# Optimization experiments

Measured on AMD Instinct MI355X. Metric: run time of the kernel, lower is better.

The kernel has to match this reference:

```python
import jax, jax.numpy as jnp
import numpy as np

D_QK = 32  # out_channels // 8


def conv1x1(x, w, b):
    # x: [B,C,H,W], w: [O,C], b: [O] -> [B,O,H,W]
    return jnp.einsum('bchw,oc->bohw', x, w) + b[None, :, None, None]


def setup_inputs() -> dict:
    key = jax.random.key(0)
    ks = jax.random.split(key, 10)
    B, C, H, W = 4, 256, 64, 64
    in_ch, out_ch, attn_ch = 512, 256, 256
    s_in = 1.0 / np.sqrt(in_ch)
    s_at = 1.0 / np.sqrt(attn_ch)
    return {
        'ef': jax.random.normal(ks[0], (B, C, H, W), jnp.float32),
        'sf': jax.random.normal(ks[1], (B, C, H, W), jnp.float32),
        'Attn': jax.random.normal(ks[2], (B, attn_ch, H, W), jnp.float32),
        'Qw': jax.random.uniform(ks[3], (D_QK, in_ch), jnp.float32, -s_in, s_in),
        'Qb': jax.random.uniform(ks[4], (D_QK,), jnp.float32, -s_in, s_in),
        'Kw': jax.random.uniform(ks[5], (D_QK, attn_ch), jnp.float32, -s_at, s_at),
        'Kb': jax.random.uniform(ks[6], (D_QK,), jnp.float32, -s_at, s_at),
        'Vw': jax.random.uniform(ks[7], (out_ch, in_ch), jnp.float32, -s_in, s_in),
        'Vb': jax.random.uniform(ks[8], (out_ch,), jnp.float32, -s_in, s_in),
        'gamma': jnp.ones((1,), jnp.float32) * 0.25,
    }


def reference(ef, sf, Attn, Qw, Qb, Kw, Kb, Vw, Vb, gamma):
    B, C, H, W = ef.shape
    N = H * W
    x = jnp.concatenate((ef, sf), axis=1)  # [B, 2C, H, W]
    q = conv1x1(x, Qw, Qb).reshape(B, D_QK, N)         # [B, d, N]
    k = conv1x1(Attn, Kw, Kb).reshape(B, D_QK, N)      # [B, d, N]
    # scores[b, m, n] = sum_d q[b, d, m] * k[b, d, n]  (no 1/sqrt(d) scale)
    scores = jnp.einsum('bdm,bdn->bmn', q, k)
    attn = jax.nn.softmax(scores, axis=-1)             # [B, N, N]
    v = conv1x1(x, Vw, Vb).reshape(B, C, N)            # [B, C, N]
    # out[b, c, m] = sum_n v[b, c, n] * attn[b, m, n]
    out = jnp.einsum('bcn,bmn->bcm', v, attn).reshape(B, C, H, W)
    return gamma[0] * out + ef
```

## Files before the change

### kernel.cpp

```cpp
#include <hip/hip_runtime.h>
#include <hip/hip_bf16.h>

typedef short bf16x8 __attribute__((ext_vector_type(8)));
typedef float f32x4 __attribute__((ext_vector_type(4)));

#define MFMA16(a, b, c) __builtin_amdgcn_mfma_f32_16x16x32_bf16(a, b, c, 0, 0, 0)

#define NB 4
#define NC 256
#define NSP 4096
#define LOG2E 1.4426950408889634f

__device__ __forceinline__ unsigned short f2bf(float f) {
    return (unsigned short)((__float_as_uint(f) + 0x8000u) >> 16);
}
__device__ __forceinline__ unsigned pk2bf(float hi, float lo) {
    return __builtin_amdgcn_perm(__float_as_uint(hi) + 0x8000u,
                                 __float_as_uint(lo) + 0x8000u, 0x07060302u);
}

__global__ __launch_bounds__(256) void prep_w(
    const float* __restrict__ Qw, const float* __restrict__ Kw,
    const float* __restrict__ Vw,
    unsigned short* __restrict__ Qwbf, unsigned short* __restrict__ Kwbf,
    unsigned short* __restrict__ Vwbf)
{
    int i = blockIdx.x * 256 + threadIdx.x;
    {
        const float4* vs = (const float4*)(Vw + (size_t)i * 8);
        float4 a = vs[0], c = vs[1];
        int4 st;
        st.x = (int)pk2bf(a.y, a.x); st.y = (int)pk2bf(a.w, a.z);
        st.z = (int)pk2bf(c.y, c.x); st.w = (int)pk2bf(c.w, c.z);
        *(int4*)(Vwbf + (size_t)i * 8) = st;
    }
    if (i < 2048) {
        const float4* qs = (const float4*)(Qw + (size_t)i * 8);
        float4 a = qs[0], c = qs[1];
        int4 st;
        st.x = (int)pk2bf(a.y, a.x); st.y = (int)pk2bf(a.w, a.z);
        st.z = (int)pk2bf(c.y, c.x); st.w = (int)pk2bf(c.w, c.z);
        *(int4*)(Qwbf + (size_t)i * 8) = st;
    }
    if (i < 1024) {
        const float4* ks = (const float4*)(Kw + (size_t)i * 8);
        float4 a = ks[0], c = ks[1];
        int4 st;
        st.x = (int)pk2bf(a.y, a.x); st.y = (int)pk2bf(a.w, a.z);
        st.z = (int)pk2bf(c.y, c.x); st.w = (int)pk2bf(c.w, c.z);
        *(int4*)(Kwbf + (size_t)i * 8) = st;
    }
}

__global__ __launch_bounds__(256) void proj_q(
    const float* __restrict__ ef, const float* __restrict__ sf,
    const unsigned short* __restrict__ Qwbf, const float* __restrict__ Qb,
    unsigned short* __restrict__ qws)
{
    __shared__ __align__(16) unsigned short xt[32][72];

    int t = threadIdx.x;
    int w = t >> 6, lane = t & 63, quad = lane >> 4, l15 = lane & 15;
    int mt = blockIdx.x, b = blockIdx.y, m0 = mt * 32;
    int ci = t & 63, sm = t >> 6;
    int mi = w >> 1, oh = w & 1;

    f32x4 acc = {0.f, 0.f, 0.f, 0.f};

    for (int c = 0; c < 8; ++c) {
        const float* src = (c < 4 ? ef : sf) +
                           ((size_t)(b * NC) + (c & 3) * 64 + ci) * NSP + m0 + sm * 8;
        float4 x0 = *(const float4*)src;
        float4 x1 = *(const float4*)(src + 4);
        __syncthreads();
        unsigned short* xd = &xt[sm * 8][ci];
        xd[0]   = f2bf(x0.x); xd[72]  = f2bf(x0.y);
        xd[144] = f2bf(x0.z); xd[216] = f2bf(x0.w);
        xd[288] = f2bf(x1.x); xd[360] = f2bf(x1.y);
        xd[432] = f2bf(x1.z); xd[504] = f2bf(x1.w);
        __syncthreads();
        int ci0 = c * 64;
#pragma unroll
        for (int ks = 0; ks < 2; ++ks) {
            bf16x8 a  = *(const bf16x8*)&xt[mi * 16 + l15][ks * 32 + quad * 8];
            bf16x8 bq = *(const bf16x8*)(Qwbf + (size_t)(oh * 16 + l15) * 512 + ci0 + ks * 32 + quad * 8);
            acc = MFMA16(a, bq, acc);
        }
    }

    int o = oh * 16 + l15;
    float bb = Qb[o];
#pragma unroll
    for (int r = 0; r < 4; ++r) {
        int m = m0 + mi * 16 + quad * 4 + r;
        qws[((size_t)(b * NSP) + m) * 32 + o] = f2bf((acc[r] + bb) * LOG2E);
    }
}

__global__ __launch_bounds__(256) void proj_k(
    const float* __restrict__ attn,
    const unsigned short* __restrict__ Kwbf, const float* __restrict__ Kb,
    unsigned short* __restrict__ kws)
{
    __shared__ __align__(16) unsigned short xt[32][72];

    int t = threadIdx.x;
    int w = t >> 6, lane = t & 63, quad = lane >> 4, l15 = lane & 15;
    int mt = blockIdx.x, b = blockIdx.y, m0 = mt * 32;
    int ci = t & 63, sm = t >> 6;
    int mi = w >> 1, oh = w & 1;

    f32x4 acc = {0.f, 0.f, 0.f, 0.f};

    for (int c = 0; c < 4; ++c) {
        const float* src = attn + ((size_t)(b * NC) + c * 64 + ci) * NSP + m0 + sm * 8;
        float4 x0 = *(const float4*)src;
        float4 x1 = *(const float4*)(src + 4);
        __syncthreads();
        unsigned short* xd = &xt[sm * 8][ci];
        xd[0]   = f2bf(x0.x); xd[72]  = f2bf(x0.y);
        xd[144] = f2bf(x0.z); xd[216] = f2bf(x0.w);
        xd[288] = f2bf(x1.x); xd[360] = f2bf(x1.y);
        xd[432] = f2bf(x1.z); xd[504] = f2bf(x1.w);
        __syncthreads();
        int ci0 = c * 64;
#pragma unroll
        for (int ks = 0; ks < 2; ++ks) {
            bf16x8 a  = *(const bf16x8*)&xt[mi * 16 + l15][ks * 32 + quad * 8];
            bf16x8 bk = *(const bf16x8*)(Kwbf + (size_t)(oh * 16 + l15) * 256 + ci0 + ks * 32 + quad * 8);
            acc = MFMA16(a, bk, acc);
        }
    }

    int o = oh * 16 + l15;
    float bb = Kb[o];
#pragma unroll
    for (int r = 0; r < 4; ++r) {
        int m = m0 + mi * 16 + quad * 4 + r;
        kws[((size_t)(b * NSP) + m) * 32 + o] = f2bf(acc[r] + bb);
    }
}

__global__ __launch_bounds__(256) void proj_v(
    const float* __restrict__ ef, const float* __restrict__ sf,
    const unsigned short* __restrict__ Vwbf, const float* __restrict__ Vb,
    unsigned short* __restrict__ vws)
{
    __shared__ __align__(16) unsigned short xt[32][72];

    int t = threadIdx.x;
    int w = t >> 6, lane = t & 63, quad = lane >> 4, l15 = lane & 15;
    int mt = blockIdx.x, b = blockIdx.y, m0 = mt * 32;
    int ci = t & 63, sm = t >> 6;

    f32x4 zero = {0.f, 0.f, 0.f, 0.f};
    f32x4 acc[2][4];
#pragma unroll
    for (int mi = 0; mi < 2; ++mi)
#pragma unroll
        for (int ot = 0; ot < 4; ++ot) acc[mi][ot] = zero;

    for (int c = 0; c < 8; ++c) {
        const float* src = (c < 4 ? ef : sf) +
                           ((size_t)(b * NC) + (c & 3) * 64 + ci) * NSP + m0 + sm * 8;
        float4 x0 = *(const float4*)src;
        float4 x1 = *(const float4*)(src + 4);
        __syncthreads();
        unsigned short* xd = &xt[sm * 8][ci];
        xd[0]   = f2bf(x0.x); xd[72]  = f2bf(x0.y);
        xd[144] = f2bf(x0.z); xd[216] = f2bf(x0.w);
        xd[288] = f2bf(x1.x); xd[360] = f2bf(x1.y);
        xd[432] = f2bf(x1.z); xd[504] = f2bf(x1.w);
        __syncthreads();
        int ci0 = c * 64;
#pragma unroll
        for (int ks = 0; ks < 2; ++ks) {
            bf16x8 a0 = *(const bf16x8*)&xt[l15][ks * 32 + quad * 8];
            bf16x8 a1 = *(const bf16x8*)&xt[16 + l15][ks * 32 + quad * 8];
#pragma unroll
            for (int ot = 0; ot < 4; ++ot) {
                bf16x8 bv = *(const bf16x8*)(Vwbf + (size_t)(w * 64 + ot * 16 + l15) * 512 + ci0 + ks * 32 + quad * 8);
                acc[0][ot] = MFMA16(a0, bv, acc[0][ot]);
                acc[1][ot] = MFMA16(a1, bv, acc[1][ot]);
            }
        }
    }

#pragma unroll
    for (int ot = 0; ot < 4; ++ot) {
        int ch = w * 64 + ot * 16 + l15;
        float bias = Vb[ch];
        unsigned* vp = (unsigned*)(vws + ((size_t)((b * 128 + mt) * 256 + ch)) * 32);
#pragma unroll
        for (int r = 0; r < 4; ++r)
            vp[quad * 4 + r] = pk2bf(acc[1][ot][r] + bias, acc[0][ot][r] + bias);
    }
}

__global__ __launch_bounds__(512, 2) void attention(
    const unsigned short* __restrict__ qws, const unsigned short* __restrict__ kws,
    const unsigned short* __restrict__ vws, const float* __restrict__ ef,
    const float* __restrict__ gamma, float* __restrict__ out)
{
    __shared__ unsigned short Plds[2][2][64 * 72];
    __shared__ float mrg[256][68];
    __shared__ float denl[2][64];

    int t = threadIdx.x;
    int g = t >> 8, tl = t & 255;
    int w = tl >> 6, lane = tl & 63, quad = lane >> 4, l15 = lane & 15;
    int b = blockIdx.x >> 6, m0 = (blockIdx.x & 63) << 6;

    const unsigned short* kbase = kws + (size_t)(b * NSP) * 32;
    const unsigned short* vbase = vws + (size_t)(b * 128) * 8192;

    bf16x8 qf = *(const bf16x8*)(qws + ((size_t)(b * NSP) + m0 + w * 16 + l15) * 32 + quad * 8);

    f32x4 zero = {0.f, 0.f, 0.f, 0.f};
    f32x4 acc[4][4];
#pragma unroll
    for (int i = 0; i < 4; ++i)
#pragma unroll
        for (int j = 0; j < 4; ++j) acc[i][j] = zero;
    float lp0 = 0.f, lp1 = 0.f, lp2 = 0.f, lp3 = 0.f;

    int tt0 = g * 64;
    bf16x8 kf[4];
#pragma unroll
    for (int j = 0; j < 4; ++j)
        kf[j] = *(const bf16x8*)(kbase + (size_t)((tt0 + (j >> 1)) * 32 + (j & 1) * 16 + l15) * 32 + quad * 8);
    bf16x8 vf[2][4];
#pragma unroll
    for (int h = 0; h < 2; ++h)
#pragma unroll
        for (int cc = 0; cc < 4; ++cc)
            vf[h][cc] = *(const bf16x8*)(vbase + (size_t)(tt0 + h) * 8192 + (w * 64 + cc * 16 + l15) * 32 + quad * 8);

    for (int it = 0; it < 32; ++it) {
        int buf = it & 1;
        f32x4 s0 = MFMA16(qf, kf[0], zero);
        f32x4 s1 = MFMA16(qf, kf[1], zero);
        f32x4 s2 = MFMA16(qf, kf[2], zero);
        f32x4 s3 = MFMA16(qf, kf[3], zero);

        float e0[4], e1[4], e2[4], e3[4];
#pragma unroll
        for (int r = 0; r < 4; ++r) {
            e0[r] = __builtin_amdgcn_exp2f(s0[r]);
            e1[r] = __builtin_amdgcn_exp2f(s1[r]);
            e2[r] = __builtin_amdgcn_exp2f(s2[r]);
            e3[r] = __builtin_amdgcn_exp2f(s3[r]);
        }
        lp0 += (e0[0] + e1[0]) + (e2[0] + e3[0]);
        lp1 += (e0[1] + e1[1]) + (e2[1] + e3[1]);
        lp2 += (e0[2] + e1[2]) + (e2[2] + e3[2]);
        lp3 += (e0[3] + e1[3]) + (e2[3] + e3[3]);

        unsigned short* pd = &Plds[g][buf][(w * 16 + quad * 4) * 72 + 2 * l15];
#pragma unroll
        for (int r = 0; r < 4; ++r) {
            *(unsigned*)(pd + r * 72)      = pk2bf(e1[r], e0[r]);
            *(unsigned*)(pd + r * 72 + 32) = pk2bf(e3[r], e2[r]);
        }

        int itn = it + 1 < 32 ? it + 1 : 31;
        int ttn = tt0 + 2 * itn;
#pragma unroll
        for (int j = 0; j < 4; ++j)
            kf[j] = *(const bf16x8*)(kbase + (size_t)((ttn + (j >> 1)) * 32 + (j & 1) * 16 + l15) * 32 + quad * 8);
        bf16x8 vfn[2][4];
#pragma unroll
        for (int h = 0; h < 2; ++h)
#pragma unroll
            for (int cc = 0; cc < 4; ++cc)
                vfn[h][cc] = *(const bf16x8*)(vbase + (size_t)(ttn + h) * 8192 + (w * 64 + cc * 16 + l15) * 32 + quad * 8);

        __syncthreads();

#pragma unroll
        for (int h = 0; h < 2; ++h) {
            bf16x8 pa0 = *(const bf16x8*)&Plds[g][buf][(0  + l15) * 72 + h * 32 + quad * 8];
            bf16x8 pa1 = *(const bf16x8*)&Plds[g][buf][(16 + l15) * 72 + h * 32 + quad * 8];
            bf16x8 pa2 = *(const bf16x8*)&Plds[g][buf][(32 + l15) * 72 + h * 32 + quad * 8];
            bf16x8 pa3 = *(const bf16x8*)&Plds[g][buf][(48 + l15) * 72 + h * 32 + quad * 8];
#pragma unroll
            for (int cc = 0; cc < 4; ++cc) {
                acc[0][cc] = MFMA16(pa0, vf[h][cc], acc[0][cc]);
                acc[1][cc] = MFMA16(pa1, vf[h][cc], acc[1][cc]);
                acc[2][cc] = MFMA16(pa2, vf[h][cc], acc[2][cc]);
                acc[3][cc] = MFMA16(pa3, vf[h][cc], acc[3][cc]);
            }
        }
#pragma unroll
        for (int h = 0; h < 2; ++h)
#pragma unroll
            for (int cc = 0; cc < 4; ++cc) vf[h][cc] = vfn[h][cc];
    }

    lp0 += __shfl_xor(lp0, 1); lp0 += __shfl_xor(lp0, 2); lp0 += __shfl_xor(lp0, 4); lp0 += __shfl_xor(lp0, 8);
    lp1 += __shfl_xor(lp1, 1); lp1 += __shfl_xor(lp1, 2); lp1 += __shfl_xor(lp1, 4); lp1 += __shfl_xor(lp1, 8);
    lp2 += __shfl_xor(lp2, 1); lp2 += __shfl_xor(lp2, 2); lp2 += __shfl_xor(lp2, 4); lp2 += __shfl_xor(lp2, 8);
    lp3 += __shfl_xor(lp3, 1); lp3 += __shfl_xor(lp3, 2); lp3 += __shfl_xor(lp3, 4); lp3 += __shfl_xor(lp3, 8);
    if (l15 == 0) {
        int base = w * 16 + quad * 4;
        denl[g][base + 0] = lp0; denl[g][base + 1] = lp1;
        denl[g][base + 2] = lp2; denl[g][base + 3] = lp3;
    }
    if (g == 1) {
#pragma unroll
        for (int qc = 0; qc < 4; ++qc)
#pragma unroll
            for (int cc = 0; cc < 4; ++cc)
                *(f32x4*)&mrg[w * 64 + cc * 16 + l15][qc * 16 + quad * 4] = acc[qc][cc];
    }
    __syncthreads();

    if (g == 0) {
        float gam = gamma[0];
#pragma unroll
        for (int qc = 0; qc < 4; ++qc) {
            int qb = qc * 16 + quad * 4;
            float4 d0 = *(const float4*)&denl[0][qb];
            float4 d1 = *(const float4*)&denl[1][qb];
            float r0 = gam / (d0.x + d1.x), r1 = gam / (d0.y + d1.y);
            float r2 = gam / (d0.z + d1.z), r3 = gam / (d0.w + d1.w);
#pragma unroll
            for (int cc = 0; cc < 4; ++cc) {
                int ch = w * 64 + cc * 16 + l15;
                f32x4 part = *(const f32x4*)&mrg[ch][qb];
                size_t off = ((size_t)(b * NC + ch)) * NSP + m0 + qb;
                float4 e = *(const float4*)(ef + off);
                float4 o;
                o.x = (acc[qc][cc][0] + part[0]) * r0 + e.x;
                o.y = (acc[qc][cc][1] + part[1]) * r1 + e.y;
                o.z = (acc[qc][cc][2] + part[2]) * r2 + e.z;
                o.w = (acc[qc][cc][3] + part[3]) * r3 + e.w;
                *(float4*)(out + off) = o;
            }
        }
    }
}

extern "C" void kernel_launch(void* const* d_in, const int* in_sizes, int n_in,
                              void* d_out, int out_size, void* d_ws, size_t ws_size,
                              hipStream_t stream) {
    const float* ef    = (const float*)d_in[0];
    const float* sf    = (const float*)d_in[1];
    const float* attn  = (const float*)d_in[2];
    const float* Qw    = (const float*)d_in[3];
    const float* Qb    = (const float*)d_in[4];
    const float* Kw    = (const float*)d_in[5];
    const float* Kb    = (const float*)d_in[6];
    const float* Vw    = (const float*)d_in[7];
    const float* Vb    = (const float*)d_in[8];
    const float* gamma = (const float*)d_in[9];
    float* out = (float*)d_out;

    unsigned short* qws  = (unsigned short*)d_ws;
    unsigned short* kws  = qws + (size_t)4 * 4096 * 32;
    unsigned short* vws  = kws + (size_t)4 * 4096 * 32;
    unsigned short* Qwbf = vws + (size_t)4 * 128 * 256 * 32;
    unsigned short* Kwbf = Qwbf + 32 * 512;
    unsigned short* Vwbf = Kwbf + 32 * 256;

    hipLaunchKernelGGL(prep_w, dim3(64), dim3(256), 0, stream,
                       Qw, Kw, Vw, Qwbf, Kwbf, Vwbf);
    hipLaunchKernelGGL(proj_q, dim3(128, 4), dim3(256), 0, stream,
                       ef, sf, Qwbf, Qb, qws);
    hipLaunchKernelGGL(proj_k, dim3(128, 4), dim3(256), 0, stream,
                       attn, Kwbf, Kb, kws);
    hipLaunchKernelGGL(proj_v, dim3(128, 4), dim3(256), 0, stream,
                       ef, sf, Vwbf, Vb, vws);
    hipLaunchKernelGGL(attention, dim3(256), dim3(512), 0, stream,
                       qws, kws, vws, ef, gamma, out);
}
```

Measured before the change: 192.0 us.

## Fuse Q/V projections, prefetch inputs, split attention keys across four groups

Merges the Q and V projection kernels so ef/sf are read and converted to bf16 once, and adds register prefetch of the next channel chunk in the projection loops. The attention kernel grows to 1024 threads, with four warp groups each covering a quarter of the key range, and combines their partial sums through a two-stage LDS reduction that reuses the P buffer. It also raises wave priority around the PV MFMA block. The gain is more parallelism per block and less redundant input traffic, at the cost of higher register and LDS pressure and extra reduction syncs.

```diff
diff --git a/kernel.cpp b/kernel.cpp
--- a/kernel.cpp
+++ b/kernel.cpp
@@ -52,10 +52,11 @@
     }
 }
 
-__global__ __launch_bounds__(256) void proj_q(
+__global__ __launch_bounds__(256) void proj_qv(
     const float* __restrict__ ef, const float* __restrict__ sf,
     const unsigned short* __restrict__ Qwbf, const float* __restrict__ Qb,
-    unsigned short* __restrict__ qws)
+    const unsigned short* __restrict__ Vwbf, const float* __restrict__ Vb,
+    unsigned short* __restrict__ qws, unsigned short* __restrict__ vws)
 {
     __shared__ __align__(16) unsigned short xt[32][72];
 
@@ -65,13 +66,27 @@
     int ci = t & 63, sm = t >> 6;
     int mi = w >> 1, oh = w & 1;
 
-    f32x4 acc = {0.f, 0.f, 0.f, 0.f};
+    f32x4 zero = {0.f, 0.f, 0.f, 0.f};
+    f32x4 acc[2][4];
+#pragma unroll
+    for (int m = 0; m < 2; ++m)
+#pragma unroll
+        for (int ot = 0; ot < 4; ++ot) acc[m][ot] = zero;
+    f32x4 qacc = zero;
+
+    const float* s0p = ef + ((size_t)(b * NC) + ci) * NSP + m0 + sm * 8;
+    float4 x0 = *(const float4*)s0p;
+    float4 x1 = *(const float4*)(s0p + 4);
 
     for (int c = 0; c < 8; ++c) {
-        const float* src = (c < 4 ? ef : sf) +
-                           ((size_t)(b * NC) + (c & 3) * 64 + ci) * NSP + m0 + sm * 8;
-        float4 x0 = *(const float4*)src;
-        float4 x1 = *(const float4*)(src + 4);
+        float4 n0 = x0, n1 = x1;
+        if (c < 7) {
+            int cn = c + 1;
+            const float* sn = (cn < 4 ? ef : sf) +
+                              ((size_t)(b * NC) + (cn & 3) * 64 + ci) * NSP + m0 + sm * 8;
+            n0 = *(const float4*)sn;
+            n1 = *(const float4*)(sn + 4);
+        }
         __syncthreads();
         unsigned short* xd = &xt[sm * 8][ci];
         xd[0]   = f2bf(x0.x); xd[72]  = f2bf(x0.y);
@@ -82,18 +97,38 @@
         int ci0 = c * 64;
 #pragma unroll
         for (int ks = 0; ks < 2; ++ks) {
-            bf16x8 a  = *(const bf16x8*)&xt[mi * 16 + l15][ks * 32 + quad * 8];
+            bf16x8 a0 = *(const bf16x8*)&xt[l15][ks * 32 + quad * 8];
+            bf16x8 a1 = *(const bf16x8*)&xt[16 + l15][ks * 32 + quad * 8];
             bf16x8 bq = *(const bf16x8*)(Qwbf + (size_t)(oh * 16 + l15) * 512 + ci0 + ks * 32 + quad * 8);
-            acc = MFMA16(a, bq, acc);
-        }
-    }
-
-    int o = oh * 16 + l15;
-    float bb = Qb[o];
-#pragma unroll
-    for (int r = 0; r < 4; ++r) {
-        int m = m0 + mi * 16 + quad * 4 + r;
-        qws[((size_t)(b * NSP) + m) * 32 + o] = f2bf((acc[r] + bb) * LOG2E);
+            qacc = MFMA16(mi ? a1 : a0, bq, qacc);
+#pragma unroll
+            for (int ot = 0; ot < 4; ++ot) {
+                bf16x8 bv = *(const bf16x8*)(Vwbf + (size_t)(w * 64 + ot * 16 + l15) * 512 + ci0 + ks * 32 + quad * 8);
+                acc[0][ot] = MFMA16(a0, bv, acc[0][ot]);
+                acc[1][ot] = MFMA16(a1, bv, acc[1][ot]);
+            }
+        }
+        x0 = n0; x1 = n1;
+    }
+
+#pragma unroll
+    for (int ot = 0; ot < 4; ++ot) {
+        int ch = w * 64 + ot * 16 + l15;
+        float bias = Vb[ch];
+        unsigned* vp = (unsigned*)(vws + ((size_t)((b * 128 + mt) * 256 + ch)) * 32);
+#pragma unroll
+        for (int r = 0; r < 4; ++r)
+            vp[quad * 4 + r] = pk2bf(acc[1][ot][r] + bias, acc[0][ot][r] + bias);
+    }
+
+    {
+        int o = oh * 16 + l15;
+        float bb = Qb[o];
+#pragma unroll
+        for (int r = 0; r < 4; ++r) {
+            int m = m0 + mi * 16 + quad * 4 + r;
+            qws[((size_t)(b * NSP) + m) * 32 + o] = f2bf((qacc[r] + bb) * LOG2E);
+        }
     }
 }
 
@@ -112,10 +147,17 @@
 
     f32x4 acc = {0.f, 0.f, 0.f, 0.f};
 
+    const float* s0p = attn + ((size_t)(b * NC) + ci) * NSP + m0 + sm * 8;
+    float4 x0 = *(const float4*)s0p;
+    float4 x1 = *(const float4*)(s0p + 4);
+
     for (int c = 0; c < 4; ++c) {
-        const float* src = attn + ((size_t)(b * NC) + c * 64 + ci) * NSP + m0 + sm * 8;
-        float4 x0 = *(const float4*)src;
-        float4 x1 = *(const float4*)(src + 4);
+        float4 n0 = x0, n1 = x1;
+        if (c < 3) {
+            const float* sn = attn + ((size_t)(b * NC) + (c + 1) * 64 + ci) * NSP + m0 + sm * 8;
+            n0 = *(const float4*)sn;
+            n1 = *(const float4*)(sn + 4);
+        }
         __syncthreads();
         unsigned short* xd = &xt[sm * 8][ci];
         xd[0]   = f2bf(x0.x); xd[72]  = f2bf(x0.y);
@@ -130,6 +172,7 @@
             bf16x8 bk = *(const bf16x8*)(Kwbf + (size_t)(oh * 16 + l15) * 256 + ci0 + ks * 32 + quad * 8);
             acc = MFMA16(a, bk, acc);
         }
+        x0 = n0; x1 = n1;
     }
 
     int o = oh * 16 + l15;
@@ -141,70 +184,14 @@
     }
 }
 
-__global__ __launch_bounds__(256) void proj_v(
-    const float* __restrict__ ef, const float* __restrict__ sf,
-    const unsigned short* __restrict__ Vwbf, const float* __restrict__ Vb,
-    unsigned short* __restrict__ vws)
-{
-    __shared__ __align__(16) unsigned short xt[32][72];
-
-    int t = threadIdx.x;
-    int w = t >> 6, lane = t & 63, quad = lane >> 4, l15 = lane & 15;
-    int mt = blockIdx.x, b = blockIdx.y, m0 = mt * 32;
-    int ci = t & 63, sm = t >> 6;
-
-    f32x4 zero = {0.f, 0.f, 0.f, 0.f};
-    f32x4 acc[2][4];
-#pragma unroll
-    for (int mi = 0; mi < 2; ++mi)
-#pragma unroll
-        for (int ot = 0; ot < 4; ++ot) acc[mi][ot] = zero;
-
-    for (int c = 0; c < 8; ++c) {
-        const float* src = (c < 4 ? ef : sf) +
-                           ((size_t)(b * NC) + (c & 3) * 64 + ci) * NSP + m0 + sm * 8;
-        float4 x0 = *(const float4*)src;
-        float4 x1 = *(const float4*)(src + 4);
-        __syncthreads();
-        unsigned short* xd = &xt[sm * 8][ci];
-        xd[0]   = f2bf(x0.x); xd[72]  = f2bf(x0.y);
-        xd[144] = f2bf(x0.z); xd[216] = f2bf(x0.w);
-        xd[288] = f2bf(x1.x); xd[360] = f2bf(x1.y);
-        xd[432] = f2bf(x1.z); xd[504] = f2bf(x1.w);
-        __syncthreads();
-        int ci0 = c * 64;
-#pragma unroll
-        for (int ks = 0; ks < 2; ++ks) {
-            bf16x8 a0 = *(const bf16x8*)&xt[l15][ks * 32 + quad * 8];
-            bf16x8 a1 = *(const bf16x8*)&xt[16 + l15][ks * 32 + quad * 8];
-#pragma unroll
-            for (int ot = 0; ot < 4; ++ot) {
-                bf16x8 bv = *(const bf16x8*)(Vwbf + (size_t)(w * 64 + ot * 16 + l15) * 512 + ci0 + ks * 32 + quad * 8);
-                acc[0][ot] = MFMA16(a0, bv, acc[0][ot]);
-                acc[1][ot] = MFMA16(a1, bv, acc[1][ot]);
-            }
-        }
-    }
-
-#pragma unroll
-    for (int ot = 0; ot < 4; ++ot) {
-        int ch = w * 64 + ot * 16 + l15;
-        float bias = Vb[ch];
-        unsigned* vp = (unsigned*)(vws + ((size_t)((b * 128 + mt) * 256 + ch)) * 32);
-#pragma unroll
-        for (int r = 0; r < 4; ++r)
-            vp[quad * 4 + r] = pk2bf(acc[1][ot][r] + bias, acc[0][ot][r] + bias);
-    }
-}
-
-__global__ __launch_bounds__(512, 2) void attention(
+__global__ __launch_bounds__(1024, 4) void attention(
     const unsigned short* __restrict__ qws, const unsigned short* __restrict__ kws,
     const unsigned short* __restrict__ vws, const float* __restrict__ ef,
     const float* __restrict__ gamma, float* __restrict__ out)
 {
-    __shared__ unsigned short Plds[2][2][64 * 72];
-    __shared__ float mrg[256][68];
-    __shared__ float denl[2][64];
+    __shared__ __align__(16) unsigned short PldsRaw[4][2][64 * 72];
+    __shared__ __align__(16) float mrgA[256][68];
+    __shared__ float denl[4][64];
 
     int t = threadIdx.x;
     int g = t >> 8, tl = t & 255;
@@ -224,7 +211,7 @@
         for (int j = 0; j < 4; ++j) acc[i][j] = zero;
     float lp0 = 0.f, lp1 = 0.f, lp2 = 0.f, lp3 = 0.f;
 
-    int tt0 = g * 64;
+    int tt0 = g * 32;
     bf16x8 kf[4];
 #pragma unroll
     for (int j = 0; j < 4; ++j)
@@ -236,7 +223,7 @@
         for (int cc = 0; cc < 4; ++cc)
             vf[h][cc] = *(const bf16x8*)(vbase + (size_t)(tt0 + h) * 8192 + (w * 64 + cc * 16 + l15) * 32 + quad * 8);
 
-    for (int it = 0; it < 32; ++it) {
+    for (int it = 0; it < 16; ++it) {
         int buf = it & 1;
         f32x4 s0 = MFMA16(qf, kf[0], zero);
         f32x4 s1 = MFMA16(qf, kf[1], zero);
@@ -256,14 +243,14 @@
         lp2 += (e0[2] + e1[2]) + (e2[2] + e3[2]);
         lp3 += (e0[3] + e1[3]) + (e2[3] + e3[3]);
 
-        unsigned short* pd = &Plds[g][buf][(w * 16 + quad * 4) * 72 + 2 * l15];
+        unsigned short* pd = &PldsRaw[g][buf][(w * 16 + quad * 4) * 72 + 2 * l15];
 #pragma unroll
         for (int r = 0; r < 4; ++r) {
             *(unsigned*)(pd + r * 72)      = pk2bf(e1[r], e0[r]);
             *(unsigned*)(pd + r * 72 + 32) = pk2bf(e3[r], e2[r]);
         }
 
-        int itn = it + 1 < 32 ? it + 1 : 31;
+        int itn = it + 1 < 16 ? it + 1 : 15;
         int ttn = tt0 + 2 * itn;
 #pragma unroll
         for (int j = 0; j < 4; ++j)
@@ -277,12 +264,13 @@
 
         __syncthreads();
 
+        __builtin_amdgcn_s_setprio(1);
 #pragma unroll
         for (int h = 0; h < 2; ++h) {
-            bf16x8 pa0 = *(const bf16x8*)&Plds[g][buf][(0  + l15) * 72 + h * 32 + quad * 8];
-            bf16x8 pa1 = *(const bf16x8*)&Plds[g][buf][(16 + l15) * 72 + h * 32 + quad * 8];
-            bf16x8 pa2 = *(const bf16x8*)&Plds[g][buf][(32 + l15) * 72 + h * 32 + quad * 8];
-            bf16x8 pa3 = *(const bf16x8*)&Plds[g][buf][(48 + l15) * 72 + h * 32 + quad * 8];
+            bf16x8 pa0 = *(const bf16x8*)&PldsRaw[g][buf][(0  + l15) * 72 + h * 32 + quad * 8];
+            bf16x8 pa1 = *(const bf16x8*)&PldsRaw[g][buf][(16 + l15) * 72 + h * 32 + quad * 8];
+            bf16x8 pa2 = *(const bf16x8*)&PldsRaw[g][buf][(32 + l15) * 72 + h * 32 + quad * 8];
+            bf16x8 pa3 = *(const bf16x8*)&PldsRaw[g][buf][(48 + l15) * 72 + h * 32 + quad * 8];
 #pragma unroll
             for (int cc = 0; cc < 4; ++cc) {
                 acc[0][cc] = MFMA16(pa0, vf[h][cc], acc[0][cc]);
@@ -291,6 +279,7 @@
                 acc[3][cc] = MFMA16(pa3, vf[h][cc], acc[3][cc]);
             }
         }
+        __builtin_amdgcn_s_setprio(0);
 #pragma unroll
         for (int h = 0; h < 2; ++h)
 #pragma unroll
@@ -306,12 +295,43 @@
         denl[g][base + 0] = lp0; denl[g][base + 1] = lp1;
         denl[g][base + 2] = lp2; denl[g][base + 3] = lp3;
     }
+    __syncthreads();
+
+    float (*mrgB)[68] = (float (*)[68])&PldsRaw[0][0][0];
+
     if (g == 1) {
 #pragma unroll
         for (int qc = 0; qc < 4; ++qc)
 #pragma unroll
             for (int cc = 0; cc < 4; ++cc)
-                *(f32x4*)&mrg[w * 64 + cc * 16 + l15][qc * 16 + quad * 4] = acc[qc][cc];
+                *(f32x4*)&mrgA[w * 64 + cc * 16 + l15][qc * 16 + quad * 4] = acc[qc][cc];
+    }
+    if (g == 3) {
+#pragma unroll
+        for (int qc = 0; qc < 4; ++qc)
+#pragma unroll
+            for (int cc = 0; cc < 4; ++cc)
+                *(f32x4*)&mrgB[w * 64 + cc * 16 + l15][qc * 16 + quad * 4] = acc[qc][cc];
+    }
+    __syncthreads();
+
+    if (g == 0) {
+#pragma unroll
+        for (int qc = 0; qc < 4; ++qc)
+#pragma unroll
+            for (int cc = 0; cc < 4; ++cc)
+                acc[qc][cc] += *(const f32x4*)&mrgA[w * 64 + cc * 16 + l15][qc * 16 + quad * 4];
+    }
+    if (g == 2) {
+#pragma unroll
+        for (int qc = 0; qc < 4; ++qc)
+#pragma unroll
+            for (int cc = 0; cc < 4; ++cc) {
+                int ch = w * 64 + cc * 16 + l15, qb = qc * 16 + quad * 4;
+                f32x4 v = *(const f32x4*)&mrgB[ch][qb];
+                v += acc[qc][cc];
+                *(f32x4*)&mrgB[ch][qb] = v;
+            }
     }
     __syncthreads();
 
@@ -322,12 +342,16 @@
             int qb = qc * 16 + quad * 4;
             float4 d0 = *(const float4*)&denl[0][qb];
             float4 d1 = *(const float4*)&denl[1][qb];
-            float r0 = gam / (d0.x + d1.x), r1 = gam / (d0.y + d1.y);
-            float r2 = gam / (d0.z + d1.z), r3 = gam / (d0.w + d1.w);
+            float4 d2 = *(const float4*)&denl[2][qb];
+            float4 d3 = *(const float4*)&denl[3][qb];
+            float r0 = gam / ((d0.x + d1.x) + (d2.x + d3.x));
+            float r1 = gam / ((d0.y + d1.y) + (d2.y + d3.y));
+            float r2 = gam / ((d0.z + d1.z) + (d2.z + d3.z));
+            float r3 = gam / ((d0.w + d1.w) + (d2.w + d3.w));
 #pragma unroll
             for (int cc = 0; cc < 4; ++cc) {
                 int ch = w * 64 + cc * 16 + l15;
-                f32x4 part = *(const f32x4*)&mrg[ch][qb];
+                f32x4 part = *(const f32x4*)&mrgB[ch][qb];
                 size_t off = ((size_t)(b * NC + ch)) * NSP + m0 + qb;
                 float4 e = *(const float4*)(ef + off);
                 float4 o;
@@ -365,12 +389,10 @@
 
     hipLaunchKernelGGL(prep_w, dim3(64), dim3(256), 0, stream,
                        Qw, Kw, Vw, Qwbf, Kwbf, Vwbf);
-    hipLaunchKernelGGL(proj_q, dim3(128, 4), dim3(256), 0, stream,
-                       ef, sf, Qwbf, Qb, qws);
+    hipLaunchKernelGGL(proj_qv, dim3(128, 4), dim3(256), 0, stream,
+                       ef, sf, Qwbf, Qb, Vwbf, Vb, qws, vws);
     hipLaunchKernelGGL(proj_k, dim3(128, 4), dim3(256), 0, stream,
                        attn, Kwbf, Kb, kws);
-    hipLaunchKernelGGL(proj_v, dim3(128, 4), dim3(256), 0, stream,
-                       ef, sf, Vwbf, Vb, vws);
-    hipLaunchKernelGGL(attention, dim3(256), dim3(512), 0, stream,
+    hipLaunchKernelGGL(attention, dim3(256), dim3(1024), 0, stream,
                        qws, kws, vws, ef, gamma, out);
 }
```

After: 498.7 us. 160% more time.
